# Optimization experiments

Hardware: AMD Instinct MI355X
Metric: run time of the kernel (lower is better)

## Reference

```python
import jax, jax.numpy as jnp
import numpy as np

# Static multi-scale pyramid (H, W) per level
SPATIAL_SHAPES = [(100, 100), (50, 50), (25, 25), (13, 13), (7, 7)]
D, H, L, P = 256, 8, 5, 4   # d_model, heads, levels, points
HD = D // H
B = 4
LQ = sum(h * w for h, w in SPATIAL_SHAPES)  # 13343
DFF = 2048


def layer_norm(x, g, b, eps=1e-5):
    m = x.mean(-1, keepdims=True)
    v = ((x - m) ** 2).mean(-1, keepdims=True)
    return (x - m) / jnp.sqrt(v + eps) * g + b


def ms_deform_attn_core(value, loc, attn):
    """value: [B, Lin, H, HD]; loc: [B, LQ, H, L, P, 2] in [0,1]; attn: [B, LQ, H, L, P].
    Bilinear sampling matches F.grid_sample(align_corners=False, padding_mode='zeros')."""
    out = jnp.zeros((B, H, LQ, HD), dtype=value.dtype)
    start = 0
    for lvl, (H_, W_) in enumerate(SPATIAL_SHAPES):
        val = value[:, start:start + H_ * W_]            # [B, HW, H, HD]
        start += H_ * W_
        val = val.transpose(0, 2, 1, 3)                   # [B, H, HW, HD]
        l = loc[:, :, :, lvl]                             # [B, LQ, H, P, 2]
        px = l[..., 0] * W_ - 0.5                         # grid_sample unnormalize
        py = l[..., 1] * H_ - 0.5
        x0 = jnp.floor(px)
        y0 = jnp.floor(py)
        wx1 = px - x0
        wy1 = py - y0
        x0i = x0.astype(jnp.int32)
        y0i = y0.astype(jnp.int32)
        samples = jnp.zeros((B, H, LQ, P, HD), dtype=value.dtype)
        for dy in (0, 1):
            for dx in (0, 1):
                xi = x0i + dx
                yi = y0i + dy
                w = (wx1 if dx else 1.0 - wx1) * (wy1 if dy else 1.0 - wy1)
                valid = (xi >= 0) & (xi < W_) & (yi >= 0) & (yi < H_)
                idx = jnp.clip(yi, 0, H_ - 1) * W_ + jnp.clip(xi, 0, W_ - 1)  # [B, LQ, H, P]
                idx_t = idx.transpose(0, 2, 1, 3).reshape(B, H, LQ * P)
                g = jnp.take_along_axis(val, idx_t[..., None], axis=2)        # [B, H, LQ*P, HD]
                g = g.reshape(B, H, LQ, P, HD)
                w_t = jnp.where(valid, w, 0.0).transpose(0, 2, 1, 3)          # [B, H, LQ, P]
                samples = samples + g * w_t[..., None]
        aw = attn[:, :, :, lvl].transpose(0, 2, 1, 3)     # [B, H, LQ, P]
        out = out + jnp.sum(samples * aw[..., None], axis=3)
    return out.transpose(0, 2, 1, 3).reshape(B, LQ, H * HD)


def setup_inputs() -> dict:
    key = jax.random.key(0)
    ks = jax.random.split(key, 24)
    s = 0.02
    inp = {
        'src': jax.random.normal(ks[0], (B, LQ, D), jnp.float32),
        'pos': jax.random.normal(ks[1], (B, LQ, D), jnp.float32),
        'reference_points': jax.random.uniform(ks[2], (B, LQ, L, 2), jnp.float32),
        'spatial_shapes': jnp.array(SPATIAL_SHAPES, dtype=jnp.int32),
        'level_start_index': jnp.array(np.cumsum([0] + [h * w for h, w in SPATIAL_SHAPES[:-1]]), dtype=jnp.int32),
        'W_off': jax.random.normal(ks[3], (D, H * L * P * 2), jnp.float32) * s,
        'b_off': jax.random.normal(ks[4], (H * L * P * 2,), jnp.float32) * s,
        'W_attn': jax.random.normal(ks[5], (D, H * L * P), jnp.float32) * s,
        'b_attn': jax.random.normal(ks[6], (H * L * P,), jnp.float32) * s,
        'W_val': jax.random.normal(ks[7], (D, D), jnp.float32) * s,
        'b_val': jax.random.normal(ks[8], (D,), jnp.float32) * s,
        'W_out': jax.random.normal(ks[9], (D, D), jnp.float32) * s,
        'b_out': jax.random.normal(ks[10], (D,), jnp.float32) * s,
        'g1': jnp.ones((D,), jnp.float32),
        'beta1': jnp.zeros((D,), jnp.float32),
        'W1': jax.random.normal(ks[11], (D, DFF), jnp.float32) * s,
        'bl1': jax.random.normal(ks[12], (DFF,), jnp.float32) * s,
        'W2': jax.random.normal(ks[13], (DFF, D), jnp.float32) * s,
        'bl2': jax.random.normal(ks[14], (D,), jnp.float32) * s,
        'g2': jnp.ones((D,), jnp.float32),
        'beta2': jnp.zeros((D,), jnp.float32),
    }
    return inp


def reference(src, pos, reference_points, spatial_shapes, level_start_index,
              W_off, b_off, W_attn, b_attn, W_val, b_val, W_out, b_out,
              g1, beta1, W1, bl1, W2, bl2, g2, beta2):
    q = src + pos                                                    # with_pos_embed
    off = (q @ W_off + b_off).reshape(B, LQ, H, L, P, 2)
    attn = jax.nn.softmax((q @ W_attn + b_attn).reshape(B, LQ, H, L * P), axis=-1)
    attn = attn.reshape(B, LQ, H, L, P)
    value = (src @ W_val + b_val).reshape(B, LQ, H, HD)
    # offset normalizer is (W, H) per level
    norm = jnp.array([[w, h] for h, w in SPATIAL_SHAPES], dtype=src.dtype)  # [L, 2]
    loc = reference_points[:, :, None, :, None, :] + off / norm[None, None, None, :, None, :]
    attn_out = ms_deform_attn_core(value, loc, attn) @ W_out + b_out
    x = layer_norm(src + attn_out, g1, beta1)                        # dropout = identity (eval)
    ffn = jax.nn.relu(x @ W1 + bl1) @ W2 + bl2
    return layer_norm(x + ffn, g2, beta2)
```

## Files before the change

### kernel.cpp

```cpp
#include <hip/hip_runtime.h>
#include <hip/hip_bf16.h>

typedef __bf16 bf16_t;
typedef __bf16 bf16x8 __attribute__((ext_vector_type(8)));
typedef float f32x4 __attribute__((ext_vector_type(4)));

#define B_    4
#define LQ_   13343
#define D_    256
#define H_    8
#define HD_   32
#define DFF_  2048
#define M_    (B_ * LQ_)

__device__ __forceinline__ int xcd_swz(int orig, int nwg) {
  int q = nwg >> 3, r = nwg & 7;
  int xcd = orig & 7, idx = orig >> 3;
  return (xcd < r ? xcd * (q + 1) : r * (q + 1) + (xcd - r) * q) + idx;
}

#define BM 128
#define BN 128
#define BK 32

#define MODE_F32       0
#define MODE_F32_ACC   1
#define MODE_BF16      2
#define MODE_BF16_RELU 3

__device__ __forceinline__ void gload_lds16(const void* g, void* l) {
  __builtin_amdgcn_global_load_lds(
      (const __attribute__((address_space(1))) void*)g,
      (__attribute__((address_space(3))) void*)l, 16, 0, 0);
}

template <int MODE, bool AF32>
__global__ __launch_bounds__(256) void gemm_bt(
    const void* __restrict__ Av, int lda,
    const bf16_t* __restrict__ Bt, int ldb,
    const float* __restrict__ bias,
    void* __restrict__ Cv, int ldc,
    int M, int N, int K)
{
  __shared__ alignas(16) bf16_t As[BM * BK];
  __shared__ alignas(16) bf16_t Bs[BN * BK];
  const int tid  = threadIdx.x;
  const int wave = tid >> 6, lane = tid & 63;
  const int nyb = (N + BN - 1) / BN;
  const int gid = xcd_swz(blockIdx.x, (int)gridDim.x);
  const int m0 = (gid / nyb) * BM;
  const int n0 = (gid - (gid / nyb) * nyb) * BN;
  const int wm = (wave & 1) * 64;
  const int wn = (wave >> 1) * 64;
  const int lrow = lane & 15;
  const int quad = lane >> 4;

  f32x4 acc[4][4] = {};

  const int srow = wave * 16 + (lane >> 2);
  const int scol = (lane & 3) * 8;
  const bf16_t* Ab = (const bf16_t*)Av;

  const int ar0 = min(m0 + srow,      M - 1);
  const int ar1 = min(m0 + srow + 64, M - 1);
  const int br0 = min(n0 + srow,      N - 1);
  const int br1 = min(n0 + srow + 64, N - 1);

  const int r0 = tid >> 2;
  const int kc = (tid & 3) * 8;

  for (int kt = 0; kt < K; kt += BK) {
    bf16x8 a0 = {}, a1 = {};
    if (AF32) {
      const float* Af = (const float*)Av;
      int gm0 = m0 + r0, gm1 = m0 + r0 + 64;
      if (gm0 < M) {
        const f32x4* p = (const f32x4*)(Af + (size_t)gm0 * lda + kt + kc);
        f32x4 u = p[0], w = p[1];
#pragma unroll
        for (int j = 0; j < 4; ++j) { a0[j] = (bf16_t)u[j]; a0[j + 4] = (bf16_t)w[j]; }
      }
      if (gm1 < M) {
        const f32x4* p = (const f32x4*)(Af + (size_t)gm1 * lda + kt + kc);
        f32x4 u = p[0], w = p[1];
#pragma unroll
        for (int j = 0; j < 4; ++j) { a1[j] = (bf16_t)u[j]; a1[j + 4] = (bf16_t)w[j]; }
      }
    }
    __syncthreads();
    if (AF32) {
      *(bf16x8*)(&As[r0 * BK + kc])        = a0;
      *(bf16x8*)(&As[(r0 + 64) * BK + kc]) = a1;
    } else {
      gload_lds16(Ab + (size_t)ar0 * lda + kt + scol, &As[wave * 512]);
      gload_lds16(Ab + (size_t)ar1 * lda + kt + scol, &As[2048 + wave * 512]);
    }
    gload_lds16(Bt + (size_t)br0 * ldb + kt + scol, &Bs[wave * 512]);
    gload_lds16(Bt + (size_t)br1 * ldb + kt + scol, &Bs[2048 + wave * 512]);
    __syncthreads();

    bf16x8 af[4], bfr[4];
#pragma unroll
    for (int i = 0; i < 4; ++i)
      af[i] = *(const bf16x8*)(&As[(wm + i * 16 + lrow) * BK + quad * 8]);
#pragma unroll
    for (int j = 0; j < 4; ++j)
      bfr[j] = *(const bf16x8*)(&Bs[(wn + j * 16 + lrow) * BK + quad * 8]);
#pragma unroll
    for (int i = 0; i < 4; ++i)
#pragma unroll
      for (int j = 0; j < 4; ++j)
        acc[i][j] = __builtin_amdgcn_mfma_f32_16x16x32_bf16(af[i], bfr[j], acc[i][j], 0, 0, 0);
  }

  float*  Cf = (float*)Cv;
  bf16_t* Cb = (bf16_t*)Cv;
#pragma unroll
  for (int i = 0; i < 4; ++i) {
#pragma unroll
    for (int j = 0; j < 4; ++j) {
      int gn = n0 + wn + j * 16 + lrow;
      if (gn >= N) continue;
      float bv = bias ? bias[gn] : 0.f;
#pragma unroll
      for (int r = 0; r < 4; ++r) {
        int gm = m0 + wm + i * 16 + quad * 4 + r;
        if (gm >= M) continue;
        float v = acc[i][j][r] + bv;
        size_t ci = (size_t)gm * ldc + gn;
        if (MODE == MODE_F32)          Cf[ci] = v;
        else if (MODE == MODE_F32_ACC) Cf[ci] += v;
        else if (MODE == MODE_BF16)    Cb[ci] = (bf16_t)v;
        else                           Cb[ci] = (bf16_t)(v > 0.f ? v : 0.f);
      }
    }
  }
}

__global__ __launch_bounds__(256) void gemm_qkv(
    const float* __restrict__ src, const float* __restrict__ pos,
    const bf16_t* __restrict__ Bt,
    const float* __restrict__ b_off, const float* __restrict__ b_attn,
    bf16_t* __restrict__ offb, float* __restrict__ attnb)
{
  __shared__ alignas(16) bf16_t As[BM * BK];
  __shared__ alignas(16) bf16_t Bs[BN * BK];
  const int tid  = threadIdx.x;
  const int wave = tid >> 6, lane = tid & 63;
  const int gid = xcd_swz(blockIdx.x, (int)gridDim.x);
  const int m0 = (gid >> 2) * BM;
  const int n0 = (gid & 3) * BN;
  const int wm = (wave & 1) * 64;
  const int wn = (wave >> 1) * 64;
  const int lrow = lane & 15;
  const int quad = lane >> 4;
  const int N = 480;

  f32x4 acc[4][4] = {};

  const int srow = wave * 16 + (lane >> 2);
  const int scol = (lane & 3) * 8;
  const int br0 = min(n0 + srow,      N - 1);
  const int br1 = min(n0 + srow + 64, N - 1);
  const int r0 = tid >> 2;
  const int kc = (tid & 3) * 8;

  for (int kt = 0; kt < 256; kt += BK) {
    bf16x8 a0 = {}, a1 = {};
    int gm0 = m0 + r0, gm1 = m0 + r0 + 64;
    if (gm0 < M_) {
      const f32x4* ps = (const f32x4*)(src + (size_t)gm0 * 256 + kt + kc);
      const f32x4* pp = (const f32x4*)(pos + (size_t)gm0 * 256 + kt + kc);
      f32x4 u = ps[0] + pp[0], w = ps[1] + pp[1];
#pragma unroll
      for (int j = 0; j < 4; ++j) { a0[j] = (bf16_t)u[j]; a0[j + 4] = (bf16_t)w[j]; }
    }
    if (gm1 < M_) {
      const f32x4* ps = (const f32x4*)(src + (size_t)gm1 * 256 + kt + kc);
      const f32x4* pp = (const f32x4*)(pos + (size_t)gm1 * 256 + kt + kc);
      f32x4 u = ps[0] + pp[0], w = ps[1] + pp[1];
#pragma unroll
      for (int j = 0; j < 4; ++j) { a1[j] = (bf16_t)u[j]; a1[j + 4] = (bf16_t)w[j]; }
    }
    __syncthreads();
    *(bf16x8*)(&As[r0 * BK + kc])        = a0;
    *(bf16x8*)(&As[(r0 + 64) * BK + kc]) = a1;
    gload_lds16(Bt + (size_t)br0 * 256 + kt + scol, &Bs[wave * 512]);
    gload_lds16(Bt + (size_t)br1 * 256 + kt + scol, &Bs[2048 + wave * 512]);
    __syncthreads();

    bf16x8 af[4], bfr[4];
#pragma unroll
    for (int i = 0; i < 4; ++i)
      af[i] = *(const bf16x8*)(&As[(wm + i * 16 + lrow) * BK + quad * 8]);
#pragma unroll
    for (int j = 0; j < 4; ++j)
      bfr[j] = *(const bf16x8*)(&Bs[(wn + j * 16 + lrow) * BK + quad * 8]);
#pragma unroll
    for (int i = 0; i < 4; ++i)
#pragma unroll
      for (int j = 0; j < 4; ++j)
        acc[i][j] = __builtin_amdgcn_mfma_f32_16x16x32_bf16(af[i], bfr[j], acc[i][j], 0, 0, 0);
  }

#pragma unroll
  for (int i = 0; i < 4; ++i) {
#pragma unroll
    for (int j = 0; j < 4; ++j) {
      int gn = n0 + wn + j * 16 + lrow;
      if (gn >= N) continue;
      float bv = (gn < 320) ? b_off[gn] : b_attn[gn - 320];
#pragma unroll
      for (int r = 0; r < 4; ++r) {
        int gm = m0 + wm + i * 16 + quad * 4 + r;
        if (gm >= M_) continue;
        float v = acc[i][j][r] + bv;
        if (gn < 320) offb[(size_t)gm * 320 + gn] = (bf16_t)v;
        else          attnb[(size_t)gm * 160 + gn - 320] = v;
      }
    }
  }
}

__global__ __launch_bounds__(256) void k_ffn(
    const bf16_t* __restrict__ x,
    const bf16_t* __restrict__ w1t,
    const float* __restrict__ bl1,
    const bf16_t* __restrict__ w2t,
    float* __restrict__ outf)
{
  __shared__ alignas(16) bf16_t xs[8][64 * 32];
  __shared__ alignas(16) bf16_t hs[4][64 * 32];
  __shared__ alignas(16) bf16_t wstage[256 * 32];
  const int tid  = threadIdx.x;
  const int wave = tid >> 6, lane = tid & 63;
  const int lrow = lane & 15, quad = lane >> 4;
  const int m0 = xcd_swz(blockIdx.x, (int)gridDim.x) * 64;
  const int srow = lane >> 2;
  const int scol = (lane & 3) * 8;
  const int wc0 = wave * 64;

  {
    int gr = min(m0 + wave * 16 + srow, M_ - 1);
#pragma unroll
    for (int c = 0; c < 8; ++c)
      gload_lds16(x + (size_t)gr * 256 + c * 32 + scol, &xs[c][wave * 512]);
  }

  f32x4 cacc[4][4] = {};

  for (int hc = 0; hc < 16; ++hc) {
    f32x4 hacc[4][2] = {};
    for (int kt = 0; kt < 8; ++kt) {
      __syncthreads();
#pragma unroll
      for (int c = 0; c < 2; ++c) {
        int r = c * 64 + wave * 16 + srow;
        gload_lds16(w1t + (size_t)(hc * 128 + r) * 256 + kt * 32 + scol,
                    &wstage[c * 2048 + wave * 512]);
      }
      __syncthreads();
      bf16x8 af[4], bf[2];
#pragma unroll
      for (int i = 0; i < 4; ++i)
        af[i] = *(const bf16x8*)(&xs[kt][(i * 16 + lrow) * 32 + quad * 8]);
#pragma unroll
      for (int j = 0; j < 2; ++j)
        bf[j] = *(const bf16x8*)(&wstage[(wave * 32 + j * 16 + lrow) * 32 + quad * 8]);
#pragma unroll
      for (int i = 0; i < 4; ++i)
#pragma unroll
        for (int j = 0; j < 2; ++j)
          hacc[i][j] = __builtin_amdgcn_mfma_f32_16x16x32_bf16(af[i], bf[j], hacc[i][j], 0, 0, 0);
    }
    {
      float b0 = bl1[hc * 128 + wave * 32 + lrow];
      float b1 = bl1[hc * 128 + wave * 32 + 16 + lrow];
#pragma unroll
      for (int i = 0; i < 4; ++i)
#pragma unroll
        for (int j = 0; j < 2; ++j) {
          float bb = j ? b1 : b0;
#pragma unroll
          for (int r = 0; r < 4; ++r) {
            float v = hacc[i][j][r] + bb;
            hs[wave][(i * 16 + quad * 4 + r) * 32 + j * 16 + lrow] =
                (bf16_t)(v > 0.f ? v : 0.f);
          }
        }
    }
    __syncthreads();
    for (int kt2 = 0; kt2 < 4; ++kt2) {
      if (kt2) __syncthreads();
#pragma unroll
      for (int c = 0; c < 4; ++c) {
        int r = c * 64 + wave * 16 + srow;
        gload_lds16(w2t + (size_t)r * 2048 + hc * 128 + kt2 * 32 + scol,
                    &wstage[c * 2048 + wave * 512]);
      }
      __syncthreads();
      bf16x8 af2[4], bf2[4];
#pragma unroll
      for (int i = 0; i < 4; ++i)
        af2[i] = *(const bf16x8*)(&hs[kt2][(i * 16 + lrow) * 32 + quad * 8]);
#pragma unroll
      for (int j = 0; j < 4; ++j)
        bf2[j] = *(const bf16x8*)(&wstage[(wc0 + j * 16 + lrow) * 32 + quad * 8]);
#pragma unroll
      for (int i = 0; i < 4; ++i)
#pragma unroll
        for (int j = 0; j < 4; ++j)
          cacc[i][j] = __builtin_amdgcn_mfma_f32_16x16x32_bf16(af2[i], bf2[j], cacc[i][j], 0, 0, 0);
    }
  }

#pragma unroll
  for (int i = 0; i < 4; ++i)
#pragma unroll
    for (int j = 0; j < 4; ++j)
#pragma unroll
      for (int r = 0; r < 4; ++r) {
        int gm = m0 + i * 16 + quad * 4 + r;
        if (gm < M_) outf[(size_t)gm * 256 + wc0 + j * 16 + lrow] = cacc[i][j][r];
      }
}

__global__ __launch_bounds__(256) void k_transpose_all(
    const float* __restrict__ i0, const float* __restrict__ i1,
    const float* __restrict__ i2, const float* __restrict__ i3,
    const float* __restrict__ i4, const float* __restrict__ i5,
    bf16_t* __restrict__ o0, bf16_t* __restrict__ o1, bf16_t* __restrict__ o2,
    bf16_t* __restrict__ o3, bf16_t* __restrict__ o4, bf16_t* __restrict__ o5)
{
  int bid = blockIdx.x;
  const float* in; bf16_t* out; int K, N, txn;
  if (bid < 80)        { in = i0; out = o0; K = 256;  N = 320;  txn = 10; }
  else if (bid < 120)  { in = i1; out = o1; K = 256;  N = 160;  bid -= 80;  txn = 5; }
  else if (bid < 184)  { in = i2; out = o2; K = 256;  N = 256;  bid -= 120; txn = 8; }
  else if (bid < 248)  { in = i3; out = o3; K = 256;  N = 256;  bid -= 184; txn = 8; }
  else if (bid < 760)  { in = i4; out = o4; K = 256;  N = 2048; bid -= 248; txn = 64; }
  else                 { in = i5; out = o5; K = 2048; N = 256;  bid -= 760; txn = 8; }
  const int bx = bid % txn, by = bid / txn;
  __shared__ float tile[32][33];
  const int k0 = by * 32, n0 = bx * 32;
  const int tx = threadIdx.x & 31, ty = threadIdx.x >> 5;
#pragma unroll
  for (int r = ty; r < 32; r += 8)
    tile[r][tx] = in[(size_t)(k0 + r) * N + n0 + tx];
  __syncthreads();
#pragma unroll
  for (int r = ty; r < 32; r += 8)
    out[(size_t)(n0 + r) * K + k0 + tx] = (bf16_t)tile[tx][r];
}

__global__ __launch_bounds__(256) void k_sample(
    const bf16_t* __restrict__ value,
    const bf16_t* __restrict__ off,
    const float* __restrict__ attn,
    const float* __restrict__ rp,
    bf16_t* __restrict__ core)
{
  const int Wl[5] = {100, 50, 25, 13, 7};
  const int st[5] = {0, 10000, 12500, 13125, 13294};
  __shared__ alignas(16) bf16_t s_off[8][320];
  __shared__ alignas(16) float  s_attn[8][160];
  __shared__ float s_rp[8][10];
  const int t = threadIdx.x;
  const int bq0 = xcd_swz(blockIdx.x, (int)gridDim.x) * 8;
  for (int i = t; i < 320; i += 256) {
    int q = i / 40, e = i - q * 40;
    if (bq0 + q < M_) {
      *(bf16x8*)&s_off[q][e * 8] = *(const bf16x8*)(off + (size_t)(bq0 + q) * 320 + e * 8);
      *(f32x4*)&s_attn[q][e * 4] = *(const f32x4*)(attn + (size_t)(bq0 + q) * 160 + e * 4);
    }
  }
  if (t < 80) {
    int q = t / 10, e = t - q * 10;
    if (bq0 + q < M_) s_rp[q][e] = rp[(size_t)(bq0 + q) * 10 + e];
  }
  __syncthreads();
  if (t < 64) {
    float* p = &s_attn[t >> 3][(t & 7) * 20];
    float mx = p[0];
#pragma unroll
    for (int i = 1; i < 20; ++i) mx = fmaxf(mx, p[i]);
    float e[20], sum = 0.f;
#pragma unroll
    for (int i = 0; i < 20; ++i) { e[i] = expf(p[i] - mx); sum += e[i]; }
    float inv = 1.f / sum;
#pragma unroll
    for (int i = 0; i < 20; ++i) p[i] = e[i] * inv;
  }
  __syncthreads();

  const int wq = t >> 5, s = t & 31;
  const int h = s >> 2, d0 = (s & 3) * 8;
  const int bq = bq0 + wq;
  if (bq >= M_) return;
  const int b = bq / LQ_;
  const bf16_t* vbase = value + ((size_t)b * LQ_) * 256 + h * 32 + d0;
  float acc[8] = {};
#pragma unroll
  for (int lvl = 0; lvl < 5; ++lvl) {
    const float W = (float)Wl[lvl];
    const float rx = s_rp[wq][lvl * 2], ry = s_rp[wq][lvl * 2 + 1];
#pragma unroll
    for (int p = 0; p < 4; ++p) {
      const int base = (h * 5 + lvl) * 4 + p;
      float px = rx * W + (float)s_off[wq][base * 2]     - 0.5f;
      float py = ry * W + (float)s_off[wq][base * 2 + 1] - 0.5f;
      float aw = s_attn[wq][h * 20 + lvl * 4 + p];
      float x0f = floorf(px), y0f = floorf(py);
      float wx1 = px - x0f, wy1 = py - y0f;
      int x0 = (int)x0f, y0 = (int)y0f;
#pragma unroll
      for (int dy = 0; dy < 2; ++dy) {
        int yi = y0 + dy;
        bool vy = (yi >= 0) & (yi < Wl[lvl]);
        int yc = min(max(yi, 0), Wl[lvl] - 1);
        float wy = dy ? wy1 : 1.f - wy1;
#pragma unroll
        for (int dx = 0; dx < 2; ++dx) {
          int xi = x0 + dx;
          bool vx = (xi >= 0) & (xi < Wl[lvl]);
          int xc = min(max(xi, 0), Wl[lvl] - 1);
          float cw = (vx & vy) ? aw * wy * (dx ? wx1 : 1.f - wx1) : 0.f;
          bf16x8 v = *(const bf16x8*)(vbase + (size_t)(st[lvl] + yc * Wl[lvl] + xc) * 256);
#pragma unroll
          for (int j = 0; j < 8; ++j) acc[j] += cw * (float)v[j];
        }
      }
    }
  }
  bf16x8 o;
#pragma unroll
  for (int j = 0; j < 8; ++j) o[j] = (bf16_t)acc[j];
  *(bf16x8*)(core + (size_t)bq * 256 + h * 32 + d0) = o;
}

template <typename TA, typename TR, typename TO>
__global__ __launch_bounds__(256) void k_ln4(
    const TA* __restrict__ a, const TR* __restrict__ res,
    const float* __restrict__ eb, const float* __restrict__ g,
    const float* __restrict__ beta, TO* __restrict__ out, int rows)
{
  const int wave = threadIdx.x >> 6, lane = threadIdx.x & 63;
  const int row = blockIdx.x * 4 + wave;
  if (row >= rows) return;
  const size_t base = (size_t)row * 256 + lane * 4;
  float v[4];
#pragma unroll
  for (int j = 0; j < 4; ++j) {
    v[j] = (float)a[base + j] + (float)res[base + j];
    if (eb) v[j] += eb[lane * 4 + j];
  }
  float s1 = v[0] + v[1] + v[2] + v[3];
  float s2 = v[0] * v[0] + v[1] * v[1] + v[2] * v[2] + v[3] * v[3];
#pragma unroll
  for (int o = 32; o > 0; o >>= 1) { s1 += __shfl_xor(s1, o); s2 += __shfl_xor(s2, o); }
  float m = s1 * (1.f / 256.f);
  float var = s2 * (1.f / 256.f) - m * m;
  float inv = rsqrtf(var + 1e-5f);
#pragma unroll
  for (int j = 0; j < 4; ++j)
    out[base + j] = (TO)(((v[j] - m) * inv) * g[lane * 4 + j] + beta[lane * 4 + j]);
}

extern "C" void kernel_launch(void* const* d_in, const int* in_sizes, int n_in,
                              void* d_out, int out_size, void* d_ws, size_t ws_size,
                              hipStream_t stream) {
  const float* src   = (const float*)d_in[0];
  const float* pos   = (const float*)d_in[1];
  const float* rp    = (const float*)d_in[2];
  const float* W_off = (const float*)d_in[5];
  const float* b_off = (const float*)d_in[6];
  const float* W_attn= (const float*)d_in[7];
  const float* b_attn= (const float*)d_in[8];
  const float* W_val = (const float*)d_in[9];
  const float* b_val = (const float*)d_in[10];
  const float* W_out = (const float*)d_in[11];
  const float* b_out = (const float*)d_in[12];
  const float* g1    = (const float*)d_in[13];
  const float* beta1 = (const float*)d_in[14];
  const float* W1    = (const float*)d_in[15];
  const float* bl1   = (const float*)d_in[16];
  const float* W2    = (const float*)d_in[17];
  const float* bl2   = (const float*)d_in[18];
  const float* g2    = (const float*)d_in[19];
  const float* beta2 = (const float*)d_in[20];

  char* ws = (char*)d_ws;
  const size_t SZ_TOK = (size_t)M_ * 256 * 2;
  const size_t SZ_ATT = (size_t)M_ * 160 * 4;

  size_t o = 0;
  bf16_t* wTqkv = (bf16_t*)(ws + o); o += 480 * 256 * 2;
  bf16_t* wTval = (bf16_t*)(ws + o); o += 256 * 256 * 2;
  bf16_t* wTout = (bf16_t*)(ws + o); o += 256 * 256 * 2;
  bf16_t* wT1   = (bf16_t*)(ws + o); o += 2048 * 256 * 2;
  bf16_t* wT2   = (bf16_t*)(ws + o); o += 2048 * 256 * 2;
  o = (o + 255) & ~(size_t)255;
  char* Areg = ws + o; o += SZ_TOK;
  char* Creg = ws + o; o += SZ_ATT;
  char* Dreg = ws + o; o += SZ_TOK;

  bf16_t* coreb   = (bf16_t*)Areg;
  float*  attnb   = (float*) Creg;
  bf16_t* attn_out= (bf16_t*)Creg;
  bf16_t* valb    = (bf16_t*)Dreg;
  bf16_t* xbuf    = (bf16_t*)Dreg;
  bf16_t* offb    = (bf16_t*)d_out;
  float*  outf    = (float*) d_out;

  k_transpose_all<<<dim3(1272), 256, 0, stream>>>(
      W_off, W_attn, W_val, W_out, W1, W2,
      wTqkv, wTqkv + 320 * 256, wTval, wTout, wT1, wT2);

  dim3 blk(256);
  const int gM = (M_ + BM - 1) / BM;

  gemm_qkv<<<dim3(gM * 4), blk, 0, stream>>>(src, pos, wTqkv, b_off, b_attn, offb, attnb);
  gemm_bt<MODE_BF16, true><<<dim3(gM * 2), blk, 0, stream>>>(src, 256, wTval, 256, b_val, valb, 256, M_, 256, 256);
  k_sample<<<dim3((M_ + 7) / 8), blk, 0, stream>>>(valb, offb, attnb, rp, coreb);
  gemm_bt<MODE_BF16, false><<<dim3(gM * 2), blk, 0, stream>>>(coreb, 256, wTout, 256, b_out, attn_out, 256, M_, 256, 256);
  k_ln4<float, bf16_t, bf16_t><<<dim3((M_ + 3) / 4), blk, 0, stream>>>(src, attn_out, (const float*)nullptr, g1, beta1, xbuf, M_);

  k_ffn<<<dim3((M_ + 63) / 64), blk, 0, stream>>>(xbuf, wT1, bl1, wT2, outf);

  k_ln4<bf16_t, float, float><<<dim3((M_ + 3) / 4), blk, 0, stream>>>(xbuf, outf, bl2, g2, beta2, outf, M_);
}
```

Baseline: 725.1 us.

## Double-buffer LDS staging in GEMM, QKV GEMM and fused FFN kernels

Adds ping-pong LDS buffers to the generic GEMM, the QKV projection GEMM and the fused FFN kernel. The next K-tile's global loads (async global-to-LDS and register-held fp32 A loads) are issued before the MFMA work on the current tile, which removes one barrier per iteration and overlaps memory latency with compute. In the FFN kernel the weight staging is chained across the W1 and W2 phases so the prefetch continues over the phase boundary. This costs more LDS per block, which may lower occupancy, and it drops the unused accumulate mode.

```diff
diff --git a/kernel.cpp b/kernel.cpp
--- a/kernel.cpp
+++ b/kernel.cpp
@@ -24,7 +24,6 @@
 #define BK 32
 
 #define MODE_F32       0
-#define MODE_F32_ACC   1
 #define MODE_BF16      2
 #define MODE_BF16_RELU 3
 
@@ -42,8 +41,8 @@
     void* __restrict__ Cv, int ldc,
     int M, int N, int K)
 {
-  __shared__ alignas(16) bf16_t As[BM * BK];
-  __shared__ alignas(16) bf16_t Bs[BN * BK];
+  __shared__ alignas(16) bf16_t As[2][BM * BK];
+  __shared__ alignas(16) bf16_t Bs[2][BN * BK];
   const int tid  = threadIdx.x;
   const int wave = tid >> 6, lane = tid & 63;
   const int nyb = (N + BN - 1) / BN;
@@ -55,11 +54,10 @@
   const int lrow = lane & 15;
   const int quad = lane >> 4;
 
-  f32x4 acc[4][4] = {};
-
   const int srow = wave * 16 + (lane >> 2);
   const int scol = (lane & 3) * 8;
   const bf16_t* Ab = (const bf16_t*)Av;
+  const float*  Af = (const float*)Av;
 
   const int ar0 = min(m0 + srow,      M - 1);
   const int ar1 = min(m0 + srow + 64, M - 1);
@@ -68,49 +66,72 @@
 
   const int r0 = tid >> 2;
   const int kc = (tid & 3) * 8;
-
-  for (int kt = 0; kt < K; kt += BK) {
-    bf16x8 a0 = {}, a1 = {};
-    if (AF32) {
-      const float* Af = (const float*)Av;
-      int gm0 = m0 + r0, gm1 = m0 + r0 + 64;
-      if (gm0 < M) {
-        const f32x4* p = (const f32x4*)(Af + (size_t)gm0 * lda + kt + kc);
-        f32x4 u = p[0], w = p[1];
-#pragma unroll
-        for (int j = 0; j < 4; ++j) { a0[j] = (bf16_t)u[j]; a0[j + 4] = (bf16_t)w[j]; }
-      }
-      if (gm1 < M) {
-        const f32x4* p = (const f32x4*)(Af + (size_t)gm1 * lda + kt + kc);
-        f32x4 u = p[0], w = p[1];
-#pragma unroll
-        for (int j = 0; j < 4; ++j) { a1[j] = (bf16_t)u[j]; a1[j + 4] = (bf16_t)w[j]; }
-      }
-    }
-    __syncthreads();
-    if (AF32) {
-      *(bf16x8*)(&As[r0 * BK + kc])        = a0;
-      *(bf16x8*)(&As[(r0 + 64) * BK + kc]) = a1;
-    } else {
-      gload_lds16(Ab + (size_t)ar0 * lda + kt + scol, &As[wave * 512]);
-      gload_lds16(Ab + (size_t)ar1 * lda + kt + scol, &As[2048 + wave * 512]);
-    }
-    gload_lds16(Bt + (size_t)br0 * ldb + kt + scol, &Bs[wave * 512]);
-    gload_lds16(Bt + (size_t)br1 * ldb + kt + scol, &Bs[2048 + wave * 512]);
-    __syncthreads();
-
+  const int arw0 = min(m0 + r0,      M - 1);
+  const int arw1 = min(m0 + r0 + 64, M - 1);
+
+  auto stage_async = [&](int ke, int buf) {
+    if (!AF32) {
+      gload_lds16(Ab + (size_t)ar0 * lda + ke + scol, &As[buf][wave * 512]);
+      gload_lds16(Ab + (size_t)ar1 * lda + ke + scol, &As[buf][2048 + wave * 512]);
+    }
+    gload_lds16(Bt + (size_t)br0 * ldb + ke + scol, &Bs[buf][wave * 512]);
+    gload_lds16(Bt + (size_t)br1 * ldb + ke + scol, &Bs[buf][2048 + wave * 512]);
+  };
+
+  if (AF32) {
+    const f32x4* p0 = (const f32x4*)(Af + (size_t)arw0 * lda + kc);
+    const f32x4* p1 = (const f32x4*)(Af + (size_t)arw1 * lda + kc);
+    f32x4 u0 = p0[0], w0 = p0[1], u1 = p1[0], w1 = p1[1];
+    bf16x8 a0, a1;
+#pragma unroll
+    for (int j = 0; j < 4; ++j) {
+      a0[j] = (bf16_t)u0[j]; a0[j + 4] = (bf16_t)w0[j];
+      a1[j] = (bf16_t)u1[j]; a1[j + 4] = (bf16_t)w1[j];
+    }
+    *(bf16x8*)(&As[0][r0 * BK + kc])        = a0;
+    *(bf16x8*)(&As[0][(r0 + 64) * BK + kc]) = a1;
+  }
+  stage_async(0, 0);
+  __syncthreads();
+
+  f32x4 acc[4][4] = {};
+  const int nkt = K / BK;
+  for (int kt = 0; kt < nkt; ++kt) {
+    const int cur = kt & 1, nxt = cur ^ 1;
+    const bool more = (kt + 1) < nkt;
+    f32x4 u0 = {}, w0 = {}, u1 = {}, w1 = {};
+    if (more) {
+      const int ke = (kt + 1) * BK;
+      if (AF32) {
+        const f32x4* p0 = (const f32x4*)(Af + (size_t)arw0 * lda + ke + kc);
+        const f32x4* p1 = (const f32x4*)(Af + (size_t)arw1 * lda + ke + kc);
+        u0 = p0[0]; w0 = p0[1]; u1 = p1[0]; w1 = p1[1];
+      }
+      stage_async(ke, nxt);
+    }
     bf16x8 af[4], bfr[4];
 #pragma unroll
     for (int i = 0; i < 4; ++i)
-      af[i] = *(const bf16x8*)(&As[(wm + i * 16 + lrow) * BK + quad * 8]);
+      af[i] = *(const bf16x8*)(&As[cur][(wm + i * 16 + lrow) * BK + quad * 8]);
 #pragma unroll
     for (int j = 0; j < 4; ++j)
-      bfr[j] = *(const bf16x8*)(&Bs[(wn + j * 16 + lrow) * BK + quad * 8]);
+      bfr[j] = *(const bf16x8*)(&Bs[cur][(wn + j * 16 + lrow) * BK + quad * 8]);
 #pragma unroll
     for (int i = 0; i < 4; ++i)
 #pragma unroll
       for (int j = 0; j < 4; ++j)
         acc[i][j] = __builtin_amdgcn_mfma_f32_16x16x32_bf16(af[i], bfr[j], acc[i][j], 0, 0, 0);
+    if (more && AF32) {
+      bf16x8 a0, a1;
+#pragma unroll
+      for (int j = 0; j < 4; ++j) {
+        a0[j] = (bf16_t)u0[j]; a0[j + 4] = (bf16_t)w0[j];
+        a1[j] = (bf16_t)u1[j]; a1[j + 4] = (bf16_t)w1[j];
+      }
+      *(bf16x8*)(&As[nxt][r0 * BK + kc])        = a0;
+      *(bf16x8*)(&As[nxt][(r0 + 64) * BK + kc]) = a1;
+    }
+    __syncthreads();
   }
 
   float*  Cf = (float*)Cv;
@@ -128,10 +149,9 @@
         if (gm >= M) continue;
         float v = acc[i][j][r] + bv;
         size_t ci = (size_t)gm * ldc + gn;
-        if (MODE == MODE_F32)          Cf[ci] = v;
-        else if (MODE == MODE_F32_ACC) Cf[ci] += v;
-        else if (MODE == MODE_BF16)    Cb[ci] = (bf16_t)v;
-        else                           Cb[ci] = (bf16_t)(v > 0.f ? v : 0.f);
+        if (MODE == MODE_F32)       Cf[ci] = v;
+        else if (MODE == MODE_BF16) Cb[ci] = (bf16_t)v;
+        else                        Cb[ci] = (bf16_t)(v > 0.f ? v : 0.f);
       }
     }
   }
@@ -143,8 +163,8 @@
     const float* __restrict__ b_off, const float* __restrict__ b_attn,
     bf16_t* __restrict__ offb, float* __restrict__ attnb)
 {
-  __shared__ alignas(16) bf16_t As[BM * BK];
-  __shared__ alignas(16) bf16_t Bs[BN * BK];
+  __shared__ alignas(16) bf16_t As[2][BM * BK];
+  __shared__ alignas(16) bf16_t Bs[2][BN * BK];
   const int tid  = threadIdx.x;
   const int wave = tid >> 6, lane = tid & 63;
   const int gid = xcd_swz(blockIdx.x, (int)gridDim.x);
@@ -156,51 +176,62 @@
   const int quad = lane >> 4;
   const int N = 480;
 
-  f32x4 acc[4][4] = {};
-
   const int srow = wave * 16 + (lane >> 2);
   const int scol = (lane & 3) * 8;
   const int br0 = min(n0 + srow,      N - 1);
   const int br1 = min(n0 + srow + 64, N - 1);
   const int r0 = tid >> 2;
   const int kc = (tid & 3) * 8;
-
-  for (int kt = 0; kt < 256; kt += BK) {
-    bf16x8 a0 = {}, a1 = {};
-    int gm0 = m0 + r0, gm1 = m0 + r0 + 64;
-    if (gm0 < M_) {
-      const f32x4* ps = (const f32x4*)(src + (size_t)gm0 * 256 + kt + kc);
-      const f32x4* pp = (const f32x4*)(pos + (size_t)gm0 * 256 + kt + kc);
-      f32x4 u = ps[0] + pp[0], w = ps[1] + pp[1];
-#pragma unroll
-      for (int j = 0; j < 4; ++j) { a0[j] = (bf16_t)u[j]; a0[j + 4] = (bf16_t)w[j]; }
-    }
-    if (gm1 < M_) {
-      const f32x4* ps = (const f32x4*)(src + (size_t)gm1 * 256 + kt + kc);
-      const f32x4* pp = (const f32x4*)(pos + (size_t)gm1 * 256 + kt + kc);
-      f32x4 u = ps[0] + pp[0], w = ps[1] + pp[1];
-#pragma unroll
-      for (int j = 0; j < 4; ++j) { a1[j] = (bf16_t)u[j]; a1[j + 4] = (bf16_t)w[j]; }
-    }
-    __syncthreads();
-    *(bf16x8*)(&As[r0 * BK + kc])        = a0;
-    *(bf16x8*)(&As[(r0 + 64) * BK + kc]) = a1;
-    gload_lds16(Bt + (size_t)br0 * 256 + kt + scol, &Bs[wave * 512]);
-    gload_lds16(Bt + (size_t)br1 * 256 + kt + scol, &Bs[2048 + wave * 512]);
-    __syncthreads();
-
+  const int arw0 = min(m0 + r0,      M_ - 1);
+  const int arw1 = min(m0 + r0 + 64, M_ - 1);
+
+  auto stageB = [&](int ke, int buf) {
+    gload_lds16(Bt + (size_t)br0 * 256 + ke + scol, &Bs[buf][wave * 512]);
+    gload_lds16(Bt + (size_t)br1 * 256 + ke + scol, &Bs[buf][2048 + wave * 512]);
+  };
+  auto loadA = [&](int ke, f32x4& u0, f32x4& w0, f32x4& u1, f32x4& w1) {
+    const f32x4* s0 = (const f32x4*)(src + (size_t)arw0 * 256 + ke + kc);
+    const f32x4* p0 = (const f32x4*)(pos + (size_t)arw0 * 256 + ke + kc);
+    const f32x4* s1 = (const f32x4*)(src + (size_t)arw1 * 256 + ke + kc);
+    const f32x4* p1 = (const f32x4*)(pos + (size_t)arw1 * 256 + ke + kc);
+    u0 = s0[0] + p0[0]; w0 = s0[1] + p0[1];
+    u1 = s1[0] + p1[0]; w1 = s1[1] + p1[1];
+  };
+  auto writeA = [&](int buf, f32x4 u0, f32x4 w0, f32x4 u1, f32x4 w1) {
+    bf16x8 a0, a1;
+#pragma unroll
+    for (int j = 0; j < 4; ++j) {
+      a0[j] = (bf16_t)u0[j]; a0[j + 4] = (bf16_t)w0[j];
+      a1[j] = (bf16_t)u1[j]; a1[j + 4] = (bf16_t)w1[j];
+    }
+    *(bf16x8*)(&As[buf][r0 * BK + kc])        = a0;
+    *(bf16x8*)(&As[buf][(r0 + 64) * BK + kc]) = a1;
+  };
+
+  { f32x4 u0, w0, u1, w1; loadA(0, u0, w0, u1, w1); writeA(0, u0, w0, u1, w1); }
+  stageB(0, 0);
+  __syncthreads();
+
+  f32x4 acc[4][4] = {};
+  for (int kt = 0; kt < 8; ++kt) {
+    const int cur = kt & 1, nxt = cur ^ 1;
+    const bool more = kt < 7;
+    f32x4 u0 = {}, w0 = {}, u1 = {}, w1 = {};
+    if (more) { loadA((kt + 1) * BK, u0, w0, u1, w1); stageB((kt + 1) * BK, nxt); }
     bf16x8 af[4], bfr[4];
 #pragma unroll
     for (int i = 0; i < 4; ++i)
-      af[i] = *(const bf16x8*)(&As[(wm + i * 16 + lrow) * BK + quad * 8]);
+      af[i] = *(const bf16x8*)(&As[cur][(wm + i * 16 + lrow) * BK + quad * 8]);
 #pragma unroll
     for (int j = 0; j < 4; ++j)
-      bfr[j] = *(const bf16x8*)(&Bs[(wn + j * 16 + lrow) * BK + quad * 8]);
+      bfr[j] = *(const bf16x8*)(&Bs[cur][(wn + j * 16 + lrow) * BK + quad * 8]);
 #pragma unroll
     for (int i = 0; i < 4; ++i)
 #pragma unroll
       for (int j = 0; j < 4; ++j)
         acc[i][j] = __builtin_amdgcn_mfma_f32_16x16x32_bf16(af[i], bfr[j], acc[i][j], 0, 0, 0);
+    if (more) writeA(nxt, u0, w0, u1, w1);
+    __syncthreads();
   }
 
 #pragma unroll
@@ -231,7 +262,7 @@
 {
   __shared__ alignas(16) bf16_t xs[8][64 * 32];
   __shared__ alignas(16) bf16_t hs[4][64 * 32];
-  __shared__ alignas(16) bf16_t wstage[256 * 32];
+  __shared__ alignas(16) bf16_t wst[2][256 * 32];
   const int tid  = threadIdx.x;
   const int wave = tid >> 6, lane = tid & 63;
   const int lrow = lane & 15, quad = lane >> 4;
@@ -240,77 +271,89 @@
   const int scol = (lane & 3) * 8;
   const int wc0 = wave * 64;
 
+  auto stage_w1 = [&](int hc, int kt, int buf) {
+#pragma unroll
+    for (int c = 0; c < 2; ++c) {
+      int r = c * 64 + wave * 16 + srow;
+      gload_lds16(w1t + (size_t)(hc * 128 + r) * 256 + kt * 32 + scol,
+                  &wst[buf][c * 2048 + wave * 512]);
+    }
+  };
+  auto stage_w2 = [&](int hc, int kt2, int buf) {
+#pragma unroll
+    for (int c = 0; c < 4; ++c) {
+      int r = c * 64 + wave * 16 + srow;
+      gload_lds16(w2t + (size_t)r * 2048 + hc * 128 + kt2 * 32 + scol,
+                  &wst[buf][c * 2048 + wave * 512]);
+    }
+  };
+
   {
     int gr = min(m0 + wave * 16 + srow, M_ - 1);
 #pragma unroll
     for (int c = 0; c < 8; ++c)
       gload_lds16(x + (size_t)gr * 256 + c * 32 + scol, &xs[c][wave * 512]);
   }
+  stage_w1(0, 0, 0);
+  __syncthreads();
 
   f32x4 cacc[4][4] = {};
-
+  int s = 0;
   for (int hc = 0; hc < 16; ++hc) {
+    float b0 = bl1[hc * 128 + wave * 32 + lrow];
+    float b1 = bl1[hc * 128 + wave * 32 + 16 + lrow];
     f32x4 hacc[4][2] = {};
     for (int kt = 0; kt < 8; ++kt) {
-      __syncthreads();
-#pragma unroll
-      for (int c = 0; c < 2; ++c) {
-        int r = c * 64 + wave * 16 + srow;
-        gload_lds16(w1t + (size_t)(hc * 128 + r) * 256 + kt * 32 + scol,
-                    &wstage[c * 2048 + wave * 512]);
-      }
-      __syncthreads();
+      const int cur = s & 1, nxt = cur ^ 1;
+      if (kt < 7) stage_w1(hc, kt + 1, nxt);
+      else        stage_w2(hc, 0, nxt);
       bf16x8 af[4], bf[2];
 #pragma unroll
       for (int i = 0; i < 4; ++i)
         af[i] = *(const bf16x8*)(&xs[kt][(i * 16 + lrow) * 32 + quad * 8]);
 #pragma unroll
       for (int j = 0; j < 2; ++j)
-        bf[j] = *(const bf16x8*)(&wstage[(wave * 32 + j * 16 + lrow) * 32 + quad * 8]);
+        bf[j] = *(const bf16x8*)(&wst[cur][(wave * 32 + j * 16 + lrow) * 32 + quad * 8]);
 #pragma unroll
       for (int i = 0; i < 4; ++i)
 #pragma unroll
         for (int j = 0; j < 2; ++j)
           hacc[i][j] = __builtin_amdgcn_mfma_f32_16x16x32_bf16(af[i], bf[j], hacc[i][j], 0, 0, 0);
-    }
-    {
-      float b0 = bl1[hc * 128 + wave * 32 + lrow];
-      float b1 = bl1[hc * 128 + wave * 32 + 16 + lrow];
-#pragma unroll
-      for (int i = 0; i < 4; ++i)
-#pragma unroll
-        for (int j = 0; j < 2; ++j) {
-          float bb = j ? b1 : b0;
-#pragma unroll
-          for (int r = 0; r < 4; ++r) {
-            float v = hacc[i][j][r] + bb;
-            hs[wave][(i * 16 + quad * 4 + r) * 32 + j * 16 + lrow] =
-                (bf16_t)(v > 0.f ? v : 0.f);
+      if (kt == 7) {
+#pragma unroll
+        for (int i = 0; i < 4; ++i)
+#pragma unroll
+          for (int j = 0; j < 2; ++j) {
+            float bb = j ? b1 : b0;
+#pragma unroll
+            for (int r = 0; r < 4; ++r) {
+              float v = hacc[i][j][r] + bb;
+              hs[wave][(i * 16 + quad * 4 + r) * 32 + j * 16 + lrow] =
+                  (bf16_t)(v > 0.f ? v : 0.f);
+            }
           }
-        }
-    }
-    __syncthreads();
+      }
+      __syncthreads();
+      ++s;
+    }
     for (int kt2 = 0; kt2 < 4; ++kt2) {
-      if (kt2) __syncthreads();
-#pragma unroll
-      for (int c = 0; c < 4; ++c) {
-        int r = c * 64 + wave * 16 + srow;
-        gload_lds16(w2t + (size_t)r * 2048 + hc * 128 + kt2 * 32 + scol,
-                    &wstage[c * 2048 + wave * 512]);
-      }
-      __syncthreads();
+      const int cur = s & 1, nxt = cur ^ 1;
+      if (kt2 < 3)      stage_w2(hc, kt2 + 1, nxt);
+      else if (hc < 15) stage_w1(hc + 1, 0, nxt);
       bf16x8 af2[4], bf2[4];
 #pragma unroll
       for (int i = 0; i < 4; ++i)
         af2[i] = *(const bf16x8*)(&hs[kt2][(i * 16 + lrow) * 32 + quad * 8]);
 #pragma unroll
       for (int j = 0; j < 4; ++j)
-        bf2[j] = *(const bf16x8*)(&wstage[(wc0 + j * 16 + lrow) * 32 + quad * 8]);
+        bf2[j] = *(const bf16x8*)(&wst[cur][(wc0 + j * 16 + lrow) * 32 + quad * 8]);
 #pragma unroll
       for (int i = 0; i < 4; ++i)
 #pragma unroll
         for (int j = 0; j < 4; ++j)
           cacc[i][j] = __builtin_amdgcn_mfma_f32_16x16x32_bf16(af2[i], bf2[j], cacc[i][j], 0, 0, 0);
+      __syncthreads();
+      ++s;
     }
   }
 
```

Result: no change. 711.4 us (-1.9%).
